# Kernel tuning notes

Measured on AMD Instinct MI355X. Metric: run time of the kernel, lower is better.

Reference implementation:

```python
import jax, jax.numpy as jnp
import numpy as np

B, S, HID, NH, HD, NL = 2, 4096, 1024, 16, 64, 128
N_ITER = 6


def setup_inputs() -> dict:
    key = jax.random.key(0)
    ks = jax.random.split(key, 9)
    s = 0.02
    D = NH * HD
    return {
        "X": jax.random.normal(ks[0], (B, S, HID), jnp.float32),
        "mask": jnp.ones((B, S), jnp.float32),
        "Wq": jax.random.normal(ks[1], (HID, D), jnp.float32) * s,
        "bq": jnp.zeros((D,), jnp.float32),
        "Wk": jax.random.normal(ks[2], (HID, D), jnp.float32) * s,
        "bk": jnp.zeros((D,), jnp.float32),
        "Wv": jax.random.normal(ks[3], (HID, D), jnp.float32) * s,
        "bv": jnp.zeros((D,), jnp.float32),
        "Wo": jax.random.normal(ks[4], (D, HID), jnp.float32) * s,
        "bo": jnp.zeros((HID,), jnp.float32),
    }


def iterative_inv(mat, n_iter=N_ITER):
    # Newton-Schulz style pseudo-inverse iteration (Nystromformer 'original' init)
    I = jnp.eye(mat.shape[-1], dtype=mat.dtype)
    K = mat
    V = K.swapaxes(-1, -2) / jnp.max(jnp.sum(K, axis=-2))
    for _ in range(n_iter):
        KV = K @ V
        V = 0.25 * V @ (13.0 * I - KV @ (15.0 * I - KV @ (7.0 * I - KV)))
    return V


def nystrom_core(Q, K, V, mask):
    # Q,K,V: [B,NH,S,HD], mask: [B,S]
    scale = 1.0 / np.sqrt(np.sqrt(HD))  # 1/d^(1/4) applied to both Q and K
    m = mask[:, None, :, None]
    Q = Q * m * scale
    K = K * m * scale
    seg = S // NL
    # landmarks: mean over contiguous segments -> [B,NH,NL,HD]
    Ql = Q.reshape(B, NH, NL, seg, HD).mean(axis=-2)
    Kl = K.reshape(B, NH, NL, seg, HD).mean(axis=-2)
    k1 = jax.nn.softmax(jnp.einsum('bhsd,bhld->bhsl', Q, Kl), axis=-1)   # [B,NH,S,NL]
    k2 = jax.nn.softmax(jnp.einsum('bhld,bhmd->bhlm', Ql, Kl), axis=-1)  # [B,NH,NL,NL]
    k3 = jax.nn.softmax(
        jnp.einsum('bhld,bhsd->bhls', Ql, K) - 1e9 * (1.0 - mask[:, None, None, :]),
        axis=-1)                                                          # [B,NH,NL,S]
    return k1 @ iterative_inv(k2) @ (k3 @ V)                              # [B,NH,S,HD]


def reference(X, mask, Wq, bq, Wk, bk, Wv, bv, Wo, bo):
    def split(Y):  # [B,S,NH*HD] -> [B,NH,S,HD]
        return Y.reshape(B, S, NH, HD).transpose(0, 2, 1, 3)
    Q = split(X @ Wq + bq)
    K = split(X @ Wk + bk)
    V = split(X @ Wv + bv)
    attn = nystrom_core(Q.astype(jnp.float32), K.astype(jnp.float32),
                        V.astype(jnp.float32), mask.astype(jnp.float32))
    out = attn.transpose(0, 2, 1, 3).reshape(B, S, NH * HD)
    return out @ Wo + bo
```

## Files before the change

### kernel.cpp

```cpp
#include <hip/hip_runtime.h>
#include <math.h>

constexpr int cB = 2, cS = 4096, cHID = 1024, cNH = 16, cHD = 64, cNL = 128, cSEG = 32, cD = 1024, cBH = 32;
constexpr float cSCALE = 0.35355339059327373f;

typedef _Float16 f16x8 __attribute__((ext_vector_type(8)));
typedef float f32x4 __attribute__((ext_vector_type(4)));

__device__ inline void gload_lds16(const void* g, void* l) {
    __builtin_amdgcn_global_load_lds(
        (const __attribute__((address_space(1))) void*)g,
        (__attribute__((address_space(3))) void*)l, 16, 0, 0);
}

__global__ __launch_bounds__(256) void cast_x(const float* __restrict__ X, _Float16* __restrict__ Xh)
{
    int i = (blockIdx.x * 256 + threadIdx.x) * 4;
    float4 v = *reinterpret_cast<const float4*>(X + i);
    union { _Float16 h[4]; ushort4 u; } p;
    p.h[0] = (_Float16)v.x; p.h[1] = (_Float16)v.y; p.h[2] = (_Float16)v.z; p.h[3] = (_Float16)v.w;
    *reinterpret_cast<ushort4*>(Xh + i) = p.u;
}

__global__ __launch_bounds__(256) void wcast_t(
    const float* __restrict__ Wq, const float* __restrict__ Wk,
    const float* __restrict__ Wv, const float* __restrict__ Wo,
    _Float16* __restrict__ WqT, _Float16* __restrict__ WkT,
    _Float16* __restrict__ WvT, _Float16* __restrict__ WoT)
{
    __shared__ float tile[32][33];
    const int wsel = blockIdx.z;
    const float* W = (wsel == 0) ? Wq : (wsel == 1 ? Wk : (wsel == 2 ? Wv : Wo));
    _Float16* WT   = (wsel == 0) ? WqT : (wsel == 1 ? WkT : (wsel == 2 ? WvT : WoT));
    const int n0 = blockIdx.x * 32, k0 = blockIdx.y * 32;
    const int t = threadIdx.x;
    const int r = t >> 3, c = (t & 7) * 4;
    float4 v = *reinterpret_cast<const float4*>(W + (size_t)(k0 + r) * cD + n0 + c);
    tile[r][c] = v.x; tile[r][c + 1] = v.y; tile[r][c + 2] = v.z; tile[r][c + 3] = v.w;
    __syncthreads();
    union { _Float16 h[4]; ushort4 u; } p;
    p.h[0] = (_Float16)tile[c + 0][r]; p.h[1] = (_Float16)tile[c + 1][r];
    p.h[2] = (_Float16)tile[c + 2][r]; p.h[3] = (_Float16)tile[c + 3][r];
    *reinterpret_cast<ushort4*>(WT + (size_t)(n0 + r) * cHID + k0 + c) = p.u;
}

__global__ __launch_bounds__(256) void xm_kernel(
    const float* __restrict__ X, const float* __restrict__ mask,
    float* __restrict__ Xm, float* __restrict__ mbar)
{
    const int bl = blockIdx.x;
    const int b = bl >> 7, l = bl & 127;
    const int c = threadIdx.x * 4;
    float4 a = {0.f, 0.f, 0.f, 0.f};
    float msum = 0.f;
    for (int j = 0; j < cSEG; ++j) {
        float m = mask[b * cS + l * cSEG + j];
        float4 x = *reinterpret_cast<const float4*>(X + ((size_t)(b * cS + l * cSEG + j)) * cHID + c);
        a.x += m * x.x; a.y += m * x.y; a.z += m * x.z; a.w += m * x.w;
        msum += m;
    }
    const float inv = 1.0f / cSEG;
    a.x *= inv; a.y *= inv; a.z *= inv; a.w *= inv;
    *reinterpret_cast<float4*>(Xm + (size_t)bl * cHID + c) = a;
    if (threadIdx.x == 0) mbar[bl] = msum * inv;
}

__global__ __launch_bounds__(256) void qkv_gemm_f16(
    const _Float16* __restrict__ Xh, const float* __restrict__ mask,
    const _Float16* __restrict__ WqT, const _Float16* __restrict__ WkT, const _Float16* __restrict__ WvT,
    const float* __restrict__ bq, const float* __restrict__ bk, const float* __restrict__ bv,
    _Float16* __restrict__ Qh, _Float16* __restrict__ Kh, _Float16* __restrict__ Vh)
{
    __shared__ __align__(16) _Float16 As[128 * 64];
    __shared__ __align__(16) _Float16 Bs[128 * 64];
    const int wsel = blockIdx.z;
    const _Float16* WT = (wsel == 0) ? WqT : (wsel == 1 ? WkT : WvT);
    const float* bias  = (wsel == 0) ? bq  : (wsel == 1 ? bk  : bv);
    _Float16* Y        = (wsel == 0) ? Qh  : (wsel == 1 ? Kh  : Vh);
    const int n0 = blockIdx.x * 128, m0 = blockIdx.y * 128;
    const int t = threadIdx.x;
    const int wave = t >> 6, lane = t & 63;
    const int wm = (wave >> 1) * 64, wn = (wave & 1) * 64;
    const int quad = lane >> 4, l15 = lane & 15;
    const int srow = wave * 8 + (lane >> 3);
    const int scol = (lane & 7) * 8;

    f32x4 acc[4][4];
#pragma unroll
    for (int i = 0; i < 4; ++i)
#pragma unroll
        for (int j = 0; j < 4; ++j) acc[i][j] = (f32x4){0.f, 0.f, 0.f, 0.f};

    for (int k0 = 0; k0 < cHID; k0 += 64) {
        const _Float16* aSrc = Xh + (size_t)(m0 + srow) * cHID + k0 + scol;
        const _Float16* bSrc = WT + (size_t)(n0 + srow) * cHID + k0 + scol;
#pragma unroll
        for (int i = 0; i < 4; ++i) {
            gload_lds16(aSrc + (size_t)(i * 32) * cHID, &As[(wave * 8 + i * 32) * 64]);
            gload_lds16(bSrc + (size_t)(i * 32) * cHID, &Bs[(wave * 8 + i * 32) * 64]);
        }
        __syncthreads();
        f16x8 af[2][4], bf[2][4];
#pragma unroll
        for (int kh = 0; kh < 2; ++kh) {
#pragma unroll
            for (int mt = 0; mt < 4; ++mt)
                af[kh][mt] = *reinterpret_cast<const f16x8*>(&As[(wm + mt * 16 + l15) * 64 + kh * 32 + quad * 8]);
#pragma unroll
            for (int nt = 0; nt < 4; ++nt)
                bf[kh][nt] = *reinterpret_cast<const f16x8*>(&Bs[(wn + nt * 16 + l15) * 64 + kh * 32 + quad * 8]);
        }
#pragma unroll
        for (int kh = 0; kh < 2; ++kh)
#pragma unroll
            for (int mt = 0; mt < 4; ++mt)
#pragma unroll
                for (int nt = 0; nt < 4; ++nt)
                    acc[mt][nt] = __builtin_amdgcn_mfma_f32_16x16x32_f16(af[kh][mt], bf[kh][nt], acc[mt][nt], 0, 0, 0);
        __syncthreads();
    }
#pragma unroll
    for (int mt = 0; mt < 4; ++mt) {
#pragma unroll
        for (int r = 0; r < 4; ++r) {
            int R = m0 + wm + mt * 16 + quad * 4 + r;
            int b = R >> 12, s = R & (cS - 1);
            float msc = (wsel < 2) ? mask[b * cS + s] * cSCALE : 1.0f;
#pragma unroll
            for (int nt = 0; nt < 4; ++nt) {
                int Cc = n0 + wn + nt * 16 + l15;
                int h = Cc >> 6, d = Cc & 63;
                float val = (acc[mt][nt][r] + bias[Cc]) * msc;
                Y[((size_t)(b * cNH + h) * cS + s) * cHD + d] = (_Float16)val;
            }
        }
    }
}

__global__ __launch_bounds__(256) void out_gemm_f16(
    const _Float16* __restrict__ Ah, const _Float16* __restrict__ WT,
    const float* __restrict__ bias, float* __restrict__ Y)
{
    __shared__ __align__(16) _Float16 As[128 * 64];
    __shared__ __align__(16) _Float16 Bs[128 * 64];
    const int n0 = blockIdx.x * 128, m0 = blockIdx.y * 128;
    const int t = threadIdx.x;
    const int wave = t >> 6, lane = t & 63;
    const int wm = (wave >> 1) * 64, wn = (wave & 1) * 64;
    const int quad = lane >> 4, l15 = lane & 15;
    const int srow = wave * 8 + (lane >> 3);
    const int scol = (lane & 7) * 8;

    f32x4 acc[4][4];
#pragma unroll
    for (int i = 0; i < 4; ++i)
#pragma unroll
        for (int j = 0; j < 4; ++j) acc[i][j] = (f32x4){0.f, 0.f, 0.f, 0.f};

    for (int k0 = 0; k0 < cD; k0 += 64) {
        const _Float16* aSrc = Ah + (size_t)(m0 + srow) * cD + k0 + scol;
        const _Float16* bSrc = WT + (size_t)(n0 + srow) * cD + k0 + scol;
#pragma unroll
        for (int i = 0; i < 4; ++i) {
            gload_lds16(aSrc + (size_t)(i * 32) * cD, &As[(wave * 8 + i * 32) * 64]);
            gload_lds16(bSrc + (size_t)(i * 32) * cD, &Bs[(wave * 8 + i * 32) * 64]);
        }
        __syncthreads();
        f16x8 af[2][4], bf[2][4];
#pragma unroll
        for (int kh = 0; kh < 2; ++kh) {
#pragma unroll
            for (int mt = 0; mt < 4; ++mt)
                af[kh][mt] = *reinterpret_cast<const f16x8*>(&As[(wm + mt * 16 + l15) * 64 + kh * 32 + quad * 8]);
#pragma unroll
            for (int nt = 0; nt < 4; ++nt)
                bf[kh][nt] = *reinterpret_cast<const f16x8*>(&Bs[(wn + nt * 16 + l15) * 64 + kh * 32 + quad * 8]);
        }
#pragma unroll
        for (int kh = 0; kh < 2; ++kh)
#pragma unroll
            for (int mt = 0; mt < 4; ++mt)
#pragma unroll
                for (int nt = 0; nt < 4; ++nt)
                    acc[mt][nt] = __builtin_amdgcn_mfma_f32_16x16x32_f16(af[kh][mt], bf[kh][nt], acc[mt][nt], 0, 0, 0);
        __syncthreads();
    }
#pragma unroll
    for (int mt = 0; mt < 4; ++mt) {
#pragma unroll
        for (int r = 0; r < 4; ++r) {
            int R = m0 + wm + mt * 16 + quad * 4 + r;
#pragma unroll
            for (int nt = 0; nt < 4; ++nt) {
                int Cc = n0 + wn + nt * 16 + l15;
                Y[(size_t)R * cHID + Cc] = acc[mt][nt][r] + bias[Cc];
            }
        }
    }
}

__global__ __launch_bounds__(256) void lgemm(
    const float* __restrict__ Xm, const float* __restrict__ mbar,
    const float* __restrict__ Wq, const float* __restrict__ bq,
    const float* __restrict__ Wk, const float* __restrict__ bk,
    float* __restrict__ Ql, float* __restrict__ Kl,
    _Float16* __restrict__ Qlh, _Float16* __restrict__ Klh)
{
    __shared__ __align__(16) float As[16][68];
    __shared__ __align__(16) float Bs[16][68];
    const int tid = threadIdx.x;
    const int wsel = blockIdx.z;
    const float* W    = wsel ? Wk : Wq;
    const float* bias = wsel ? bk : bq;
    float* Yl         = wsel ? Kl : Ql;
    _Float16* Ylh     = wsel ? Klh : Qlh;
    const int c0 = blockIdx.x * 64, r0 = blockIdx.y * 64;
    const int tx = tid & 15, ty = tid >> 4;
    const int am = tid >> 2, ak = (tid & 3) * 4;
    const int bkk = tid >> 4, bn = (tid & 15) * 4;

    float acc[4][4] = {};
    for (int k0 = 0; k0 < cHID; k0 += 16) {
        float4 a4 = *reinterpret_cast<const float4*>(Xm + (size_t)(r0 + am) * cHID + k0 + ak);
        As[ak + 0][am] = a4.x; As[ak + 1][am] = a4.y; As[ak + 2][am] = a4.z; As[ak + 3][am] = a4.w;
        float4 b4 = *reinterpret_cast<const float4*>(W + (size_t)(k0 + bkk) * cD + c0 + bn);
        *reinterpret_cast<float4*>(&Bs[bkk][bn]) = b4;
        __syncthreads();
#pragma unroll
        for (int kk = 0; kk < 16; ++kk) {
            float4 av  = *reinterpret_cast<const float4*>(&As[kk][ty * 4]);
            float4 bv4 = *reinterpret_cast<const float4*>(&Bs[kk][tx * 4]);
            float a_[4] = {av.x, av.y, av.z, av.w};
            float b_[4] = {bv4.x, bv4.y, bv4.z, bv4.w};
#pragma unroll
            for (int i = 0; i < 4; ++i)
#pragma unroll
                for (int j = 0; j < 4; ++j) acc[i][j] += a_[i] * b_[j];
        }
        __syncthreads();
    }
#pragma unroll
    for (int i = 0; i < 4; ++i) {
        int r = r0 + ty * 4 + i;
        int b = r >> 7, l = r & 127;
        float mb = mbar[r];
#pragma unroll
        for (int j = 0; j < 4; ++j) {
            int c = c0 + tx * 4 + j;
            int h = c >> 6, d = c & 63;
            float val = (acc[i][j] + mb * bias[c]) * cSCALE;
            size_t idx = ((size_t)(b * cNH + h) * cNL + l) * cHD + d;
            Yl[idx] = val;
            Ylh[idx] = (_Float16)val;
        }
    }
}

__global__ __launch_bounds__(128) void k2_softmax(
    const float* __restrict__ Ql, const float* __restrict__ Kl, float* __restrict__ k2)
{
    __shared__ __align__(16) float qrow[64];
    __shared__ float red[128];
    int bh = blockIdx.x >> 7, i = blockIdx.x & 127;
    int j = threadIdx.x;
    if (j < 64) qrow[j] = Ql[(bh * cNL + i) * cHD + j];
    __syncthreads();
    const float4* q4  = reinterpret_cast<const float4*>(qrow);
    const float4* kl4 = reinterpret_cast<const float4*>(Kl + (bh * cNL + j) * cHD);
    float dot = 0.f;
#pragma unroll
    for (int u = 0; u < 16; ++u) {
        float4 a = q4[u], b = kl4[u];
        dot += a.x * b.x + a.y * b.y + a.z * b.z + a.w * b.w;
    }
    red[j] = dot; __syncthreads();
    for (int off = 64; off > 0; off >>= 1) { if (j < off) red[j] = fmaxf(red[j], red[j + off]); __syncthreads(); }
    float m = red[0]; __syncthreads();
    float e = expf(dot - m);
    red[j] = e; __syncthreads();
    for (int off = 64; off > 0; off >>= 1) { if (j < off) red[j] += red[j + off]; __syncthreads(); }
    k2[(bh * cNL + i) * cNL + j] = e / red[0];
}

__global__ __launch_bounds__(128) void colsum_max(const float* __restrict__ k2, int* __restrict__ cmax)
{
    __shared__ float red[128];
    int bh = blockIdx.x, j = threadIdx.x;
    float s = 0.f;
    for (int i = 0; i < cNL; ++i) s += k2[(bh * cNL + i) * cNL + j];
    red[j] = s; __syncthreads();
    for (int off = 64; off > 0; off >>= 1) { if (j < off) red[j] = fmaxf(red[j], red[j + off]); __syncthreads(); }
    if (j == 0) atomicMax(cmax, __float_as_int(red[0]));
}

__device__ inline unsigned int packsplit(float v) {
    _Float16 h = (_Float16)v;
    _Float16 l = (_Float16)(v - (float)h);
    union { _Float16 f; unsigned short u; } ha, la;
    ha.f = h; la.f = l;
    return ((unsigned int)ha.u << 16) | (unsigned int)la.u;
}
__device__ inline float h2f(unsigned short u) {
    union { unsigned short u; _Float16 f; } c; c.u = u; return (float)c.f;
}

#define NYS_PRODUCT(Rbuf, LH, LL)                                                       \
    {                                                                                   \
        _Pragma("unroll")                                                               \
        for (int nt_ = 0; nt_ < 8; ++nt_) {                                             \
            f32x4 a_ = (f32x4){0.f, 0.f, 0.f, 0.f};                                     \
            _Pragma("unroll")                                                           \
            for (int k0_ = 0; k0_ < 4; ++k0_) {                                         \
                const unsigned int* p_ = Rbuf + (nt_ * 16 + l15) * 132 + k0_ * 32 + quad * 8; \
                uint4 w0_ = *reinterpret_cast<const uint4*>(p_);                        \
                uint4 w1_ = *reinterpret_cast<const uint4*>(p_ + 4);                    \
                union { f16x8 v; unsigned int u[4]; } bh_, bl_;                         \
                bh_.u[0] = (w0_.x >> 16) | (w0_.y & 0xFFFF0000u);                       \
                bh_.u[1] = (w0_.z >> 16) | (w0_.w & 0xFFFF0000u);                       \
                bh_.u[2] = (w1_.x >> 16) | (w1_.y & 0xFFFF0000u);                       \
                bh_.u[3] = (w1_.z >> 16) | (w1_.w & 0xFFFF0000u);                       \
                bl_.u[0] = (w0_.x & 0xFFFFu) | (w0_.y << 16);                           \
                bl_.u[1] = (w0_.z & 0xFFFFu) | (w0_.w << 16);                           \
                bl_.u[2] = (w1_.x & 0xFFFFu) | (w1_.y << 16);                           \
                bl_.u[3] = (w1_.z & 0xFFFFu) | (w1_.w << 16);                           \
                a_ = __builtin_amdgcn_mfma_f32_16x16x32_f16(LH[k0_], bh_.v, a_, 0, 0, 0); \
                a_ = __builtin_amdgcn_mfma_f32_16x16x32_f16(LL[k0_], bh_.v, a_, 0, 0, 0); \
                a_ = __builtin_amdgcn_mfma_f32_16x16x32_f16(LH[k0_], bl_.v, a_, 0, 0, 0); \
            }                                                                           \
            acc[nt_] = a_;                                                              \
        }                                                                               \
    }

#define NYS_SCATTER(Rbuf, alphav)                                                       \
    {                                                                                   \
        _Pragma("unroll")                                                               \
        for (int nt_ = 0; nt_ < 8; ++nt_) {                                             \
            _Pragma("unroll")                                                           \
            for (int r_ = 0; r_ < 4; ++r_) {                                            \
                int row_ = wave * 16 + quad * 4 + r_;                                   \
                int col_ = nt_ * 16 + l15;                                              \
                float v_ = -acc[nt_][r_];                                               \
                if (row_ == col_) v_ += (alphav);                                       \
                Rbuf[col_ * 132 + row_] = packsplit(v_);                                \
            }                                                                           \
        }                                                                               \
    }

__global__ __launch_bounds__(512, 2) void nys_fused(
    const float* __restrict__ k2, const int* __restrict__ cmax, float* __restrict__ V6)
{
    __shared__ __align__(16) unsigned int RT0[128 * 132];
    __shared__ __align__(16) unsigned int RT1[128 * 132];
    const int bh = blockIdx.x;
    const int t = threadIdx.x;
    const int wave = t >> 6, lane = t & 63;
    const int quad = lane >> 4, l15 = lane & 15;
    const int rowL = wave * 16 + l15;
    const float* Kg = k2 + (size_t)bh * (cNL * cNL);
    const float invc = 1.0f / __int_as_float(*cmax);

#pragma unroll
    for (int i = 0; i < 32; ++i) {
        int idx = t + i * 512;
        RT0[(idx >> 7) * 132 + (idx & 127)] = packsplit(Kg[idx] * invc);
    }

    f16x8 Khi[4], Klo[4];
#pragma unroll
    for (int k0 = 0; k0 < 4; ++k0) {
        const float* src = Kg + (size_t)rowL * cNL + k0 * 32 + quad * 8;
        union { f16x8 v; unsigned short s[8]; } hh, ll;
#pragma unroll
        for (int j = 0; j < 8; ++j) {
            float v = src[j];
            _Float16 h = (_Float16)v;
            _Float16 l = (_Float16)(v - (float)h);
            union { _Float16 f; unsigned short u; } cb;
            cb.f = h; hh.s[j] = cb.u;
            cb.f = l; ll.s[j] = cb.u;
        }
        Khi[k0] = hh.v; Klo[k0] = ll.v;
    }
    __syncthreads();

    f32x4 acc[8];
    f16x8 Ahi[4], Alo[4], Vhi[4], Vlo[4];

    for (int it = 0; it < 6; ++it) {
        NYS_PRODUCT(RT0, Khi, Klo);
        __syncthreads();
        NYS_SCATTER(RT1, 7.0f);
        __syncthreads();

#pragma unroll
        for (int k0 = 0; k0 < 4; ++k0) {
            union { f16x8 v; unsigned short s[8]; } hh, ll;
#pragma unroll
            for (int j = 0; j < 8; ++j) {
                int kk = k0 * 32 + quad * 8 + j;
                unsigned int u = RT1[kk * 132 + rowL];
                float val = h2f((unsigned short)(u >> 16)) + h2f((unsigned short)(u & 0xFFFFu));
                float a = (kk == rowL) ? (7.0f - val) : (-val);
                _Float16 h = (_Float16)a;
                _Float16 l = (_Float16)(a - (float)h);
                union { _Float16 f; unsigned short u2; } cb;
                cb.f = h; hh.s[j] = cb.u2;
                cb.f = l; ll.s[j] = cb.u2;
            }
            Ahi[k0] = hh.v; Alo[k0] = ll.v;
        }

        NYS_PRODUCT(RT1, Ahi, Alo);
        __syncthreads();
        NYS_SCATTER(RT1, 15.0f);
        __syncthreads();

        NYS_PRODUCT(RT1, Ahi, Alo);

#pragma unroll
        for (int k0 = 0; k0 < 4; ++k0) {
            union { f16x8 v; unsigned short s[8]; } hh, ll;
#pragma unroll
            for (int j = 0; j < 8; ++j) {
                unsigned int u = RT0[(k0 * 32 + quad * 8 + j) * 132 + rowL];
                hh.s[j] = (unsigned short)(u >> 16);
                ll.s[j] = (unsigned short)(u & 0xFFFFu);
            }
            Vhi[k0] = hh.v; Vlo[k0] = ll.v;
        }
        __syncthreads();
        NYS_SCATTER(RT1, 13.0f);
        __syncthreads();

        NYS_PRODUCT(RT1, Vhi, Vlo);
        if (it < 5) {
            __syncthreads();
#pragma unroll
            for (int nt = 0; nt < 8; ++nt)
#pragma unroll
                for (int r = 0; r < 4; ++r) {
                    int row = wave * 16 + quad * 4 + r;
                    int col = nt * 16 + l15;
                    RT0[col * 132 + row] = packsplit(0.25f * acc[nt][r]);
                }
            __syncthreads();
        }
    }
#pragma unroll
    for (int nt = 0; nt < 8; ++nt)
#pragma unroll
        for (int r = 0; r < 4; ++r) {
            int row = wave * 16 + quad * 4 + r;
            int col = nt * 16 + l15;
            V6[(size_t)bh * (cNL * cNL) + row * cNL + col] = 0.25f * acc[nt][r];
        }
}

__global__ __launch_bounds__(256) void vtrans(const _Float16* __restrict__ Vh, _Float16* __restrict__ VTh)
{
    __shared__ ushort T[64][72];
    const int s0 = blockIdx.x * 64, bh = blockIdx.y;
    const int t = threadIdx.x;
    const _Float16* vb = Vh + ((size_t)bh * cS + s0) * cHD;
#pragma unroll
    for (int i = 0; i < 2; ++i) {
        int idx = t + i * 256;
        int row = idx >> 3, c8 = idx & 7;
        f16x8 v = *reinterpret_cast<const f16x8*>(vb + (size_t)row * cHD + c8 * 8);
#pragma unroll
        for (int j = 0; j < 8; ++j) T[row][c8 * 8 + j] = ((ushort*)&v)[j];
    }
    __syncthreads();
    _Float16* vt = VTh + (size_t)bh * cHD * cS;
#pragma unroll
    for (int i = 0; i < 2; ++i) {
        int idx = t + i * 256;
        int d = idx >> 3, s8 = idx & 7;
        f16x8 o;
#pragma unroll
        for (int j = 0; j < 8; ++j) ((ushort*)&o)[j] = T[s8 * 8 + j][d];
        *reinterpret_cast<f16x8*>(vt + (size_t)d * cS + s0 + s8 * 8) = o;
    }
}

__global__ __launch_bounds__(256) void k3v_mfma(
    const _Float16* __restrict__ Qlh, const _Float16* __restrict__ Kh,
    const _Float16* __restrict__ VTh, const float* __restrict__ mask,
    float* __restrict__ Opart, float* __restrict__ mpart, float* __restrict__ spart)
{
    __shared__ __align__(16) _Float16 Ps[128 * 72];
    __shared__ float msk[256];
    const int z = blockIdx.x, bh = blockIdx.y;
    const int b = bh >> 4;
    const int sbase = z * 256;
    const int t = threadIdx.x;
    const int wave = t >> 6, lane = t & 63;
    const int quad = lane >> 4, l15 = lane & 15;

    msk[t] = mask[b * cS + sbase + t];

    f16x8 aq[2][2];
    const _Float16* qlg = Qlh + (size_t)bh * cNL * cHD;
#pragma unroll
    for (int mt = 0; mt < 2; ++mt)
#pragma unroll
        for (int k0 = 0; k0 < 2; ++k0)
            aq[mt][k0] = *reinterpret_cast<const f16x8*>(
                qlg + (size_t)(wave * 32 + mt * 16 + l15) * cHD + k0 * 32 + quad * 8);

    float mrun[2][4], srun[2][4];
    f32x4 accO[2][4];
#pragma unroll
    for (int mt = 0; mt < 2; ++mt)
#pragma unroll
        for (int r = 0; r < 4; ++r) { mrun[mt][r] = -1e30f; srun[mt][r] = 0.f; }
#pragma unroll
    for (int mt = 0; mt < 2; ++mt)
#pragma unroll
        for (int dt = 0; dt < 4; ++dt) accO[mt][dt] = (f32x4){0.f, 0.f, 0.f, 0.f};

    __syncthreads();

    const _Float16* kg = Kh + (size_t)bh * cS * cHD;
    const _Float16* vg = VTh + (size_t)bh * cHD * cS;

    for (int step = 0; step < 4; ++step) {
        const int st = sbase + step * 64;
        f32x4 accS[2][4];
#pragma unroll
        for (int mt = 0; mt < 2; ++mt)
#pragma unroll
            for (int nt = 0; nt < 4; ++nt) accS[mt][nt] = (f32x4){0.f, 0.f, 0.f, 0.f};
#pragma unroll
        for (int k0 = 0; k0 < 2; ++k0)
#pragma unroll
            for (int nt = 0; nt < 4; ++nt) {
                f16x8 bk = *reinterpret_cast<const f16x8*>(
                    kg + (size_t)(st + nt * 16 + l15) * cHD + k0 * 32 + quad * 8);
#pragma unroll
                for (int mt = 0; mt < 2; ++mt)
                    accS[mt][nt] = __builtin_amdgcn_mfma_f32_16x16x32_f16(aq[mt][k0], bk, accS[mt][nt], 0, 0, 0);
            }
#pragma unroll
        for (int nt = 0; nt < 4; ++nt) {
            float pen = 1e9f * (1.0f - msk[step * 64 + nt * 16 + l15]);
#pragma unroll
            for (int mt = 0; mt < 2; ++mt)
#pragma unroll
                for (int r = 0; r < 4; ++r) accS[mt][nt][r] -= pen;
        }
#pragma unroll
        for (int mt = 0; mt < 2; ++mt) {
#pragma unroll
            for (int r = 0; r < 4; ++r) {
                float tmax = fmaxf(fmaxf(accS[mt][0][r], accS[mt][1][r]),
                                   fmaxf(accS[mt][2][r], accS[mt][3][r]));
#pragma unroll
                for (int w = 1; w < 16; w <<= 1) tmax = fmaxf(tmax, __shfl_xor(tmax, w, 16));
                float mnew = fmaxf(mrun[mt][r], tmax);
                float alpha = __expf(mrun[mt][r] - mnew);
                float ts = 0.f;
#pragma unroll
                for (int nt = 0; nt < 4; ++nt) {
                    float e = __expf(accS[mt][nt][r] - mnew);
                    accS[mt][nt][r] = e; ts += e;
                }
#pragma unroll
                for (int w = 1; w < 16; w <<= 1) ts += __shfl_xor(ts, w, 16);
                srun[mt][r] = srun[mt][r] * alpha + ts;
                mrun[mt][r] = mnew;
#pragma unroll
                for (int dt = 0; dt < 4; ++dt) accO[mt][dt][r] *= alpha;
            }
        }
#pragma unroll
        for (int mt = 0; mt < 2; ++mt)
#pragma unroll
            for (int nt = 0; nt < 4; ++nt)
#pragma unroll
                for (int r = 0; r < 4; ++r)
                    Ps[(wave * 32 + mt * 16 + quad * 4 + r) * 72 + nt * 16 + l15] =
                        (_Float16)accS[mt][nt][r];
#pragma unroll
        for (int k0 = 0; k0 < 2; ++k0) {
            f16x8 ap[2];
#pragma unroll
            for (int mt = 0; mt < 2; ++mt)
                ap[mt] = *reinterpret_cast<const f16x8*>(
                    &Ps[(wave * 32 + mt * 16 + l15) * 72 + k0 * 32 + quad * 8]);
#pragma unroll
            for (int dt = 0; dt < 4; ++dt) {
                f16x8 bv = *reinterpret_cast<const f16x8*>(
                    vg + (size_t)(dt * 16 + l15) * cS + st + k0 * 32 + quad * 8);
#pragma unroll
                for (int mt = 0; mt < 2; ++mt)
                    accO[mt][dt] = __builtin_amdgcn_mfma_f32_16x16x32_f16(ap[mt], bv, accO[mt][dt], 0, 0, 0);
            }
        }
    }
    const int rowbase = bh * cNL + wave * 32;
#pragma unroll
    for (int mt = 0; mt < 2; ++mt)
#pragma unroll
        for (int dt = 0; dt < 4; ++dt)
#pragma unroll
            for (int r = 0; r < 4; ++r)
                Opart[(size_t)(z * 4096 + rowbase + mt * 16 + quad * 4 + r) * cHD + dt * 16 + l15] =
                    accO[mt][dt][r];
    if (l15 == 0) {
#pragma unroll
        for (int mt = 0; mt < 2; ++mt)
#pragma unroll
            for (int r = 0; r < 4; ++r) {
                int prow = z * 4096 + rowbase + mt * 16 + quad * 4 + r;
                mpart[prow] = mrun[mt][r];
                spart[prow] = srun[mt][r];
            }
    }
}

__global__ __launch_bounds__(256) void k3v_reduce(
    const float* __restrict__ Opart, const float* __restrict__ mpart,
    const float* __restrict__ spart, float* __restrict__ CV)
{
    const int t = threadIdx.x;
    const int row = blockIdx.x * 4 + (t >> 6);
    const int d = t & 63;
    float mstar = -1e30f;
#pragma unroll
    for (int z = 0; z < 16; ++z) mstar = fmaxf(mstar, mpart[z * 4096 + row]);
    float ssum = 0.f, acc = 0.f;
#pragma unroll
    for (int z = 0; z < 16; ++z) {
        float w = __expf(mpart[z * 4096 + row] - mstar);
        ssum += w * spart[z * 4096 + row];
        acc  += w * Opart[(size_t)(z * 4096 + row) * cHD + d];
    }
    CV[(size_t)row * cHD + d] = acc / ssum;
}

__global__ __launch_bounds__(256) void w2_matmul(
    const float* __restrict__ V6, const float* __restrict__ CV, _Float16* __restrict__ W2T)
{
    __shared__ __align__(16) float CVs[128][64];
    const int bh = blockIdx.x, t = threadIdx.x;
    for (int k = 0; k < 32; ++k) { int idx = t + k * 256; CVs[idx >> 6][idx & 63] = CV[bh * 8192 + idx]; }
    __syncthreads();
    const int tx = t & 15, ty = t >> 4;
    float acc[8][4] = {};
    for (int k = 0; k < 128; ++k) {
        float4 b4 = *reinterpret_cast<const float4*>(&CVs[k][tx * 4]);
#pragma unroll
        for (int i = 0; i < 8; ++i) {
            float a = V6[(bh * cNL + ty * 8 + i) * cNL + k];
            acc[i][0] += a * b4.x; acc[i][1] += a * b4.y; acc[i][2] += a * b4.z; acc[i][3] += a * b4.w;
        }
    }
    _Float16* wt = W2T + (size_t)bh * cHD * cNL;
#pragma unroll
    for (int i = 0; i < 8; ++i)
#pragma unroll
        for (int j = 0; j < 4; ++j)
            wt[(size_t)(tx * 4 + j) * cNL + ty * 8 + i] = (_Float16)acc[i][j];
}

__global__ __launch_bounds__(256) void k1_mfma(
    const _Float16* __restrict__ Qh, const _Float16* __restrict__ Klh,
    const _Float16* __restrict__ W2T, _Float16* __restrict__ ctxh)
{
    __shared__ __align__(16) _Float16 Qs[64 * 72];
    __shared__ __align__(16) _Float16 Ps[64 * 136];
    const int s0 = blockIdx.x * 64, bh = blockIdx.y;
    const int b = bh >> 4, h = bh & 15;
    const int t = threadIdx.x;
    const int wave = t >> 6, lane = t & 63;
    const int quad = lane >> 4, l15 = lane & 15;

    {
        const _Float16* qg = Qh + ((size_t)bh * cS + s0) * cHD;
#pragma unroll
        for (int i = 0; i < 2; ++i) {
            int idx = t + i * 256;
            int row = idx >> 3, c8 = idx & 7;
            *reinterpret_cast<f16x8*>(&Qs[row * 72 + c8 * 8]) =
                *reinterpret_cast<const f16x8*>(qg + (size_t)row * cHD + c8 * 8);
        }
    }
    __syncthreads();

    const _Float16* klg = Klh + (size_t)bh * cNL * cHD;
    f32x4 accS[8];
#pragma unroll
    for (int nt = 0; nt < 8; ++nt) accS[nt] = (f32x4){0.f, 0.f, 0.f, 0.f};
#pragma unroll
    for (int k0 = 0; k0 < 2; ++k0) {
        f16x8 aq = *reinterpret_cast<const f16x8*>(&Qs[(wave * 16 + l15) * 72 + k0 * 32 + quad * 8]);
#pragma unroll
        for (int nt = 0; nt < 8; ++nt) {
            f16x8 bk = *reinterpret_cast<const f16x8*>(klg + (size_t)(nt * 16 + l15) * cHD + k0 * 32 + quad * 8);
            accS[nt] = __builtin_amdgcn_mfma_f32_16x16x32_f16(aq, bk, accS[nt], 0, 0, 0);
        }
    }

    float rmax[4] = {-1e30f, -1e30f, -1e30f, -1e30f};
#pragma unroll
    for (int nt = 0; nt < 8; ++nt)
#pragma unroll
        for (int r = 0; r < 4; ++r) rmax[r] = fmaxf(rmax[r], accS[nt][r]);
#pragma unroll
    for (int r = 0; r < 4; ++r)
#pragma unroll
        for (int w = 1; w < 16; w <<= 1) rmax[r] = fmaxf(rmax[r], __shfl_xor(rmax[r], w, 16));
    float rsum[4] = {0.f, 0.f, 0.f, 0.f};
#pragma unroll
    for (int nt = 0; nt < 8; ++nt)
#pragma unroll
        for (int r = 0; r < 4; ++r) { accS[nt][r] = __expf(accS[nt][r] - rmax[r]); rsum[r] += accS[nt][r]; }
#pragma unroll
    for (int r = 0; r < 4; ++r) {
#pragma unroll
        for (int w = 1; w < 16; w <<= 1) rsum[r] += __shfl_xor(rsum[r], w, 16);
        rsum[r] = 1.0f / rsum[r];
    }
#pragma unroll
    for (int nt = 0; nt < 8; ++nt)
#pragma unroll
        for (int r = 0; r < 4; ++r)
            Ps[(wave * 16 + quad * 4 + r) * 136 + nt * 16 + l15] = (_Float16)(accS[nt][r] * rsum[r]);
    __syncthreads();

    const _Float16* wtg = W2T + (size_t)bh * cHD * cNL;
    f32x4 accO[4];
#pragma unroll
    for (int nt = 0; nt < 4; ++nt) accO[nt] = (f32x4){0.f, 0.f, 0.f, 0.f};
#pragma unroll
    for (int k0 = 0; k0 < 4; ++k0) {
        f16x8 ap = *reinterpret_cast<const f16x8*>(&Ps[(wave * 16 + l15) * 136 + k0 * 32 + quad * 8]);
#pragma unroll
        for (int nt = 0; nt < 4; ++nt) {
            f16x8 bw = *reinterpret_cast<const f16x8*>(wtg + (size_t)(nt * 16 + l15) * cNL + k0 * 32 + quad * 8);
            accO[nt] = __builtin_amdgcn_mfma_f32_16x16x32_f16(ap, bw, accO[nt], 0, 0, 0);
        }
    }
#pragma unroll
    for (int nt = 0; nt < 4; ++nt)
#pragma unroll
        for (int r = 0; r < 4; ++r) {
            int s = s0 + wave * 16 + quad * 4 + r;
            int d = nt * 16 + l15;
            ctxh[((size_t)(b * cS) + s) * cD + h * cHD + d] = (_Float16)accO[nt][r];
        }
}

extern "C" void kernel_launch(void* const* d_in, const int* in_sizes, int n_in,
                              void* d_out, int out_size, void* d_ws, size_t ws_size,
                              hipStream_t stream)
{
    const float* X    = (const float*)d_in[0];
    const float* mask = (const float*)d_in[1];
    const float* Wq   = (const float*)d_in[2];
    const float* bq   = (const float*)d_in[3];
    const float* Wk   = (const float*)d_in[4];
    const float* bk   = (const float*)d_in[5];
    const float* Wv   = (const float*)d_in[6];
    const float* bv   = (const float*)d_in[7];
    const float* Wo   = (const float*)d_in[8];
    const float* bo   = (const float*)d_in[9];
    float* out = (float*)d_out;

    float* ws = (float*)d_ws;
    size_t off = 0;
    const size_t szQKV = (size_t)cBH * cS * cHD;
    const size_t szL   = (size_t)cBH * cNL * cHD;
    const size_t szM   = (size_t)cBH * cNL * cNL;
    float* Qr   = ws + off; off += szQKV;
    float* Kr   = ws + off; off += szQKV;
    float* Vr   = ws + off; off += szQKV;
    _Float16* Xh  = (_Float16*)(ws + off); off += szQKV / 2;
    _Float16* WqT = (_Float16*)(ws + off); off += 524288;
    _Float16* WkT = (_Float16*)(ws + off); off += 524288;
    _Float16* WvT = (_Float16*)(ws + off); off += 524288;
    _Float16* WoT = (_Float16*)(ws + off); off += 524288;
    float* Xm   = ws + off; off += (size_t)cB * cNL * cHID;
    float* mbar = ws + off; off += 256;
    float* Ql  = ws + off; off += szL;
    float* Kl  = ws + off; off += szL;
    float* k2  = ws + off; off += szM;
    float* Vb0 = ws + off; off += szM;
    float* Vb1 = ws + off; off += szM;
    float* Zb  = ws + off; off += szM;
    float* T2b = ws + off; off += szM;
    float* T3b = ws + off; off += szM;
    float* CV  = ws + off; off += szL;
    _Float16* Qlh  = (_Float16*)(ws + off); off += szL / 2;
    _Float16* Klh  = (_Float16*)(ws + off); off += szL / 2;
    _Float16* W2Th = (_Float16*)(ws + off); off += szL / 2;
    int*   cmax = (int*)(ws + off); off += 16;
    float* mpart = ws + off; off += 65536;
    float* spart = ws + off; off += 65536;

    _Float16* Qh   = (_Float16*)Qr;
    float*    Opart = Qr + szQKV / 2;
    _Float16* Kh   = (_Float16*)Kr;
    _Float16* ctxh = (_Float16*)(Kr + szQKV / 2);
    _Float16* Vh   = (_Float16*)Vr;
    _Float16* VTh  = (_Float16*)(Vr + szQKV / 2);

    (void)Vb1; (void)Zb; (void)T2b; (void)T3b;

    hipMemsetAsync(cmax, 0, sizeof(int), stream);

    cast_x<<<(int)(szQKV / 1024), 256, 0, stream>>>(X, Xh);
    wcast_t<<<dim3(32, 32, 4), 256, 0, stream>>>(Wq, Wk, Wv, Wo, WqT, WkT, WvT, WoT);
    xm_kernel<<<cB * cNL, 256, 0, stream>>>(X, mask, Xm, mbar);

    qkv_gemm_f16<<<dim3(cD / 128, (cB * cS) / 128, 3), 256, 0, stream>>>(
        Xh, mask, WqT, WkT, WvT, bq, bk, bv, Qh, Kh, Vh);
    vtrans<<<dim3(cS / 64, cBH), 256, 0, stream>>>(Vh, VTh);
    lgemm<<<dim3(cD / 64, (cB * cNL) / 64, 2), 256, 0, stream>>>(Xm, mbar, Wq, bq, Wk, bk, Ql, Kl, Qlh, Klh);

    k2_softmax<<<cBH * cNL, 128, 0, stream>>>(Ql, Kl, k2);
    colsum_max<<<cBH, 128, 0, stream>>>(k2, cmax);

    nys_fused<<<cBH, 512, 0, stream>>>(k2, cmax, Vb0);

    k3v_mfma<<<dim3(16, cBH), 256, 0, stream>>>(Qlh, Kh, VTh, mask, Opart, mpart, spart);
    k3v_reduce<<<1024, 256, 0, stream>>>(Opart, mpart, spart, CV);
    w2_matmul<<<cBH, 256, 0, stream>>>(Vb0, CV, W2Th);
    k1_mfma<<<dim3(cS / 64, cBH), 256, 0, stream>>>(Qh, Klh, W2Th, ctxh);
    out_gemm_f16<<<dim3(cHID / 128, (cB * cS) / 128), 256, 0, stream>>>(ctxh, WoT, bo, out);
}
```

Baseline: 514.1 us.

## Restructure Newton-Schulz kernel: split hi/lo LDS planes, 4 waves with 2 M-tiles

The fused Newton-Schulz inverse kernel now keeps the fp16 hi and lo parts in separate LDS arrays instead of packed 32-bit words, so B operands load directly as f16x8 and no longer need per-element unpacking. It runs 256 threads where each wave owns two 16-row tiles, with two independent accumulator chains interleaved to keep more MFMAs in flight. Scatter writes are vectorized ushort4 stores, and one barrier after the first product is dropped because the first product reads a different buffer. Fewer waves per block and more registers per wave may reduce latency hiding, and this kernel runs on only 32 blocks.

```diff
diff --git a/kernel.cpp b/kernel.cpp
--- a/kernel.cpp
+++ b/kernel.cpp
@@ -293,167 +293,184 @@
     if (j == 0) atomicMax(cmax, __float_as_int(red[0]));
 }
 
-__device__ inline unsigned int packsplit(float v) {
-    _Float16 h = (_Float16)v;
-    _Float16 l = (_Float16)(v - (float)h);
-    union { _Float16 f; unsigned short u; } ha, la;
-    ha.f = h; la.f = l;
-    return ((unsigned int)ha.u << 16) | (unsigned int)la.u;
-}
-__device__ inline float h2f(unsigned short u) {
-    union { unsigned short u; _Float16 f; } c; c.u = u; return (float)c.f;
-}
-
-#define NYS_PRODUCT(Rbuf, LH, LL)                                                       \
+__device__ inline void split2(float v, _Float16& h, _Float16& l) {
+    h = (_Float16)v;
+    l = (_Float16)(v - (float)h);
+}
+
+#define NYS_MFMA(a, b, c) __builtin_amdgcn_mfma_f32_16x16x32_f16((a), (b), (c), 0, 0, 0)
+
+#define NYS_PRODUCT(PH, PL, LH, LL)                                                     \
     {                                                                                   \
         _Pragma("unroll")                                                               \
         for (int nt_ = 0; nt_ < 8; ++nt_) {                                             \
-            f32x4 a_ = (f32x4){0.f, 0.f, 0.f, 0.f};                                     \
+            f32x4 a0_ = (f32x4){0.f, 0.f, 0.f, 0.f};                                    \
+            f32x4 a1_ = (f32x4){0.f, 0.f, 0.f, 0.f};                                    \
             _Pragma("unroll")                                                           \
             for (int k0_ = 0; k0_ < 4; ++k0_) {                                         \
-                const unsigned int* p_ = Rbuf + (nt_ * 16 + l15) * 132 + k0_ * 32 + quad * 8; \
-                uint4 w0_ = *reinterpret_cast<const uint4*>(p_);                        \
-                uint4 w1_ = *reinterpret_cast<const uint4*>(p_ + 4);                    \
-                union { f16x8 v; unsigned int u[4]; } bh_, bl_;                         \
-                bh_.u[0] = (w0_.x >> 16) | (w0_.y & 0xFFFF0000u);                       \
-                bh_.u[1] = (w0_.z >> 16) | (w0_.w & 0xFFFF0000u);                       \
-                bh_.u[2] = (w1_.x >> 16) | (w1_.y & 0xFFFF0000u);                       \
-                bh_.u[3] = (w1_.z >> 16) | (w1_.w & 0xFFFF0000u);                       \
-                bl_.u[0] = (w0_.x & 0xFFFFu) | (w0_.y << 16);                           \
-                bl_.u[1] = (w0_.z & 0xFFFFu) | (w0_.w << 16);                           \
-                bl_.u[2] = (w1_.x & 0xFFFFu) | (w1_.y << 16);                           \
-                bl_.u[3] = (w1_.z & 0xFFFFu) | (w1_.w << 16);                           \
-                a_ = __builtin_amdgcn_mfma_f32_16x16x32_f16(LH[k0_], bh_.v, a_, 0, 0, 0); \
-                a_ = __builtin_amdgcn_mfma_f32_16x16x32_f16(LL[k0_], bh_.v, a_, 0, 0, 0); \
-                a_ = __builtin_amdgcn_mfma_f32_16x16x32_f16(LH[k0_], bl_.v, a_, 0, 0, 0); \
+                f16x8 bh_ = *reinterpret_cast<const f16x8*>(&PH[(nt_ * 16 + l15) * 136 + k0_ * 32 + quad * 8]); \
+                f16x8 bl_ = *reinterpret_cast<const f16x8*>(&PL[(nt_ * 16 + l15) * 136 + k0_ * 32 + quad * 8]); \
+                a0_ = NYS_MFMA(LH[0][k0_], bh_, a0_);                                   \
+                a1_ = NYS_MFMA(LH[1][k0_], bh_, a1_);                                   \
+                a0_ = NYS_MFMA(LL[0][k0_], bh_, a0_);                                   \
+                a1_ = NYS_MFMA(LL[1][k0_], bh_, a1_);                                   \
+                a0_ = NYS_MFMA(LH[0][k0_], bl_, a0_);                                   \
+                a1_ = NYS_MFMA(LH[1][k0_], bl_, a1_);                                   \
             }                                                                           \
-            acc[nt_] = a_;                                                              \
+            acc[0][nt_] = a0_; acc[1][nt_] = a1_;                                       \
         }                                                                               \
     }
 
-#define NYS_SCATTER(Rbuf, alphav)                                                       \
+#define NYS_SCATTER_W(alphav)                                                           \
     {                                                                                   \
         _Pragma("unroll")                                                               \
-        for (int nt_ = 0; nt_ < 8; ++nt_) {                                             \
+        for (int mt_ = 0; mt_ < 2; ++mt_) {                                             \
             _Pragma("unroll")                                                           \
-            for (int r_ = 0; r_ < 4; ++r_) {                                            \
-                int row_ = wave * 16 + quad * 4 + r_;                                   \
+            for (int nt_ = 0; nt_ < 8; ++nt_) {                                         \
                 int col_ = nt_ * 16 + l15;                                              \
-                float v_ = -acc[nt_][r_];                                               \
-                if (row_ == col_) v_ += (alphav);                                       \
-                Rbuf[col_ * 132 + row_] = packsplit(v_);                                \
+                int rb_  = wave * 32 + mt_ * 16 + quad * 4;                             \
+                ushort4 ph_, pl_;                                                       \
+                _Pragma("unroll")                                                       \
+                for (int r_ = 0; r_ < 4; ++r_) {                                        \
+                    float v_ = ((rb_ + r_) == col_ ? (alphav) : 0.f) - acc[mt_][nt_][r_]; \
+                    _Float16 h_, l_; split2(v_, h_, l_);                                \
+                    ((unsigned short*)&ph_)[r_] = __builtin_bit_cast(unsigned short, h_); \
+                    ((unsigned short*)&pl_)[r_] = __builtin_bit_cast(unsigned short, l_); \
+                }                                                                       \
+                *reinterpret_cast<ushort4*>(&Whi_s[col_ * 136 + rb_]) = ph_;            \
+                *reinterpret_cast<ushort4*>(&Wlo_s[col_ * 136 + rb_]) = pl_;            \
             }                                                                           \
         }                                                                               \
     }
 
-__global__ __launch_bounds__(512, 2) void nys_fused(
+__global__ __launch_bounds__(256, 1) void nys_fused(
     const float* __restrict__ k2, const int* __restrict__ cmax, float* __restrict__ V6)
 {
-    __shared__ __align__(16) unsigned int RT0[128 * 132];
-    __shared__ __align__(16) unsigned int RT1[128 * 132];
+    __shared__ __align__(16) _Float16 Vhi_s[128 * 136];
+    __shared__ __align__(16) _Float16 Vlo_s[128 * 136];
+    __shared__ __align__(16) _Float16 Whi_s[128 * 136];
+    __shared__ __align__(16) _Float16 Wlo_s[128 * 136];
     const int bh = blockIdx.x;
     const int t = threadIdx.x;
     const int wave = t >> 6, lane = t & 63;
     const int quad = lane >> 4, l15 = lane & 15;
-    const int rowL = wave * 16 + l15;
     const float* Kg = k2 + (size_t)bh * (cNL * cNL);
     const float invc = 1.0f / __int_as_float(*cmax);
 
 #pragma unroll
-    for (int i = 0; i < 32; ++i) {
-        int idx = t + i * 512;
-        RT0[(idx >> 7) * 132 + (idx & 127)] = packsplit(Kg[idx] * invc);
-    }
-
-    f16x8 Khi[4], Klo[4];
-#pragma unroll
-    for (int k0 = 0; k0 < 4; ++k0) {
-        const float* src = Kg + (size_t)rowL * cNL + k0 * 32 + quad * 8;
-        union { f16x8 v; unsigned short s[8]; } hh, ll;
-#pragma unroll
-        for (int j = 0; j < 8; ++j) {
-            float v = src[j];
-            _Float16 h = (_Float16)v;
-            _Float16 l = (_Float16)(v - (float)h);
-            union { _Float16 f; unsigned short u; } cb;
-            cb.f = h; hh.s[j] = cb.u;
-            cb.f = l; ll.s[j] = cb.u;
-        }
-        Khi[k0] = hh.v; Klo[k0] = ll.v;
+    for (int i = 0; i < 16; ++i) {
+        int idx = t + i * 256;
+        int row = idx >> 5, c4 = (idx & 31) * 4;
+        float4 v = *reinterpret_cast<const float4*>(Kg + (size_t)row * cNL + c4);
+        ushort4 ph, pl;
+        _Float16 h, l;
+        split2(v.x * invc, h, l); ((unsigned short*)&ph)[0] = __builtin_bit_cast(unsigned short, h); ((unsigned short*)&pl)[0] = __builtin_bit_cast(unsigned short, l);
+        split2(v.y * invc, h, l); ((unsigned short*)&ph)[1] = __builtin_bit_cast(unsigned short, h); ((unsigned short*)&pl)[1] = __builtin_bit_cast(unsigned short, l);
+        split2(v.z * invc, h, l); ((unsigned short*)&ph)[2] = __builtin_bit_cast(unsigned short, h); ((unsigned short*)&pl)[2] = __builtin_bit_cast(unsigned short, l);
+        split2(v.w * invc, h, l); ((unsigned short*)&ph)[3] = __builtin_bit_cast(unsigned short, h); ((unsigned short*)&pl)[3] = __builtin_bit_cast(unsigned short, l);
+        *reinterpret_cast<ushort4*>(&Vhi_s[row * 136 + c4]) = ph;
+        *reinterpret_cast<ushort4*>(&Vlo_s[row * 136 + c4]) = pl;
+    }
+
+    f16x8 Khi[2][4], Klo[2][4];
+#pragma unroll
+    for (int mt = 0; mt < 2; ++mt) {
+        const int rowL = wave * 32 + mt * 16 + l15;
+#pragma unroll
+        for (int k0 = 0; k0 < 4; ++k0) {
+            const float* src = Kg + (size_t)rowL * cNL + k0 * 32 + quad * 8;
+            union { f16x8 v; _Float16 e[8]; } hh, ll;
+#pragma unroll
+            for (int j = 0; j < 8; ++j) split2(src[j], hh.e[j], ll.e[j]);
+            Khi[mt][k0] = hh.v; Klo[mt][k0] = ll.v;
+        }
     }
     __syncthreads();
 
-    f32x4 acc[8];
-    f16x8 Ahi[4], Alo[4], Vhi[4], Vlo[4];
+    f32x4 acc[2][8];
+    f16x8 Ahi[2][4], Alo[2][4];
 
     for (int it = 0; it < 6; ++it) {
-        NYS_PRODUCT(RT0, Khi, Klo);
-        __syncthreads();
-        NYS_SCATTER(RT1, 7.0f);
-        __syncthreads();
-
-#pragma unroll
-        for (int k0 = 0; k0 < 4; ++k0) {
-            union { f16x8 v; unsigned short s[8]; } hh, ll;
-#pragma unroll
-            for (int j = 0; j < 8; ++j) {
-                int kk = k0 * 32 + quad * 8 + j;
-                unsigned int u = RT1[kk * 132 + rowL];
-                float val = h2f((unsigned short)(u >> 16)) + h2f((unsigned short)(u & 0xFFFFu));
-                float a = (kk == rowL) ? (7.0f - val) : (-val);
-                _Float16 h = (_Float16)a;
-                _Float16 l = (_Float16)(a - (float)h);
-                union { _Float16 f; unsigned short u2; } cb;
-                cb.f = h; hh.s[j] = cb.u2;
-                cb.f = l; ll.s[j] = cb.u2;
-            }
-            Ahi[k0] = hh.v; Alo[k0] = ll.v;
-        }
-
-        NYS_PRODUCT(RT1, Ahi, Alo);
-        __syncthreads();
-        NYS_SCATTER(RT1, 15.0f);
-        __syncthreads();
-
-        NYS_PRODUCT(RT1, Ahi, Alo);
-
-#pragma unroll
-        for (int k0 = 0; k0 < 4; ++k0) {
-            union { f16x8 v; unsigned short s[8]; } hh, ll;
-#pragma unroll
-            for (int j = 0; j < 8; ++j) {
-                unsigned int u = RT0[(k0 * 32 + quad * 8 + j) * 132 + rowL];
-                hh.s[j] = (unsigned short)(u >> 16);
-                ll.s[j] = (unsigned short)(u & 0xFFFFu);
-            }
-            Vhi[k0] = hh.v; Vlo[k0] = ll.v;
-        }
-        __syncthreads();
-        NYS_SCATTER(RT1, 13.0f);
-        __syncthreads();
-
-        NYS_PRODUCT(RT1, Vhi, Vlo);
+        NYS_PRODUCT(Vhi_s, Vlo_s, Khi, Klo);
+        NYS_SCATTER_W(7.0f);
+        __syncthreads();
+
+#pragma unroll
+        for (int mt = 0; mt < 2; ++mt) {
+            const int rowL = wave * 32 + mt * 16 + l15;
+#pragma unroll
+            for (int k0 = 0; k0 < 4; ++k0) {
+                union { f16x8 v; _Float16 e[8]; } hh, ll;
+#pragma unroll
+                for (int j = 0; j < 8; ++j) {
+                    int kk = k0 * 32 + quad * 8 + j;
+                    float s = (float)Whi_s[kk * 136 + rowL] + (float)Wlo_s[kk * 136 + rowL];
+                    float a = ((kk == rowL) ? 7.0f : 0.0f) - s;
+                    split2(a, hh.e[j], ll.e[j]);
+                }
+                Ahi[mt][k0] = hh.v; Alo[mt][k0] = ll.v;
+            }
+        }
+
+        NYS_PRODUCT(Whi_s, Wlo_s, Ahi, Alo);
+        __syncthreads();
+        NYS_SCATTER_W(15.0f);
+        __syncthreads();
+
+        NYS_PRODUCT(Whi_s, Wlo_s, Ahi, Alo);
+
+        f16x8 Vlh[2][4], Vll[2][4];
+#pragma unroll
+        for (int mt = 0; mt < 2; ++mt) {
+            const int rowL = wave * 32 + mt * 16 + l15;
+#pragma unroll
+            for (int k0 = 0; k0 < 4; ++k0) {
+                union { f16x8 v; _Float16 e[8]; } hh, ll;
+#pragma unroll
+                for (int j = 0; j < 8; ++j) {
+                    int kk = k0 * 32 + quad * 8 + j;
+                    hh.e[j] = Vhi_s[kk * 136 + rowL];
+                    ll.e[j] = Vlo_s[kk * 136 + rowL];
+                }
+                Vlh[mt][k0] = hh.v; Vll[mt][k0] = ll.v;
+            }
+        }
+        __syncthreads();
+        NYS_SCATTER_W(13.0f);
+        __syncthreads();
+
+        NYS_PRODUCT(Whi_s, Wlo_s, Vlh, Vll);
         if (it < 5) {
+#pragma unroll
+            for (int mt = 0; mt < 2; ++mt) {
+#pragma unroll
+                for (int nt = 0; nt < 8; ++nt) {
+                    int col = nt * 16 + l15;
+                    int rb  = wave * 32 + mt * 16 + quad * 4;
+                    ushort4 ph, pl;
+#pragma unroll
+                    for (int r = 0; r < 4; ++r) {
+                        _Float16 h, l; split2(0.25f * acc[mt][nt][r], h, l);
+                        ((unsigned short*)&ph)[r] = __builtin_bit_cast(unsigned short, h);
+                        ((unsigned short*)&pl)[r] = __builtin_bit_cast(unsigned short, l);
+                    }
+                    *reinterpret_cast<ushort4*>(&Vhi_s[col * 136 + rb]) = ph;
+                    *reinterpret_cast<ushort4*>(&Vlo_s[col * 136 + rb]) = pl;
+                }
+            }
             __syncthreads();
-#pragma unroll
-            for (int nt = 0; nt < 8; ++nt)
-#pragma unroll
-                for (int r = 0; r < 4; ++r) {
-                    int row = wave * 16 + quad * 4 + r;
-                    int col = nt * 16 + l15;
-                    RT0[col * 132 + row] = packsplit(0.25f * acc[nt][r]);
-                }
-            __syncthreads();
-        }
-    }
-#pragma unroll
-    for (int nt = 0; nt < 8; ++nt)
-#pragma unroll
-        for (int r = 0; r < 4; ++r) {
-            int row = wave * 16 + quad * 4 + r;
-            int col = nt * 16 + l15;
-            V6[(size_t)bh * (cNL * cNL) + row * cNL + col] = 0.25f * acc[nt][r];
-        }
+        }
+    }
+#pragma unroll
+    for (int mt = 0; mt < 2; ++mt)
+#pragma unroll
+        for (int nt = 0; nt < 8; ++nt)
+#pragma unroll
+            for (int r = 0; r < 4; ++r) {
+                int row = wave * 32 + mt * 16 + quad * 4 + r;
+                int col = nt * 16 + l15;
+                V6[(size_t)bh * (cNL * cNL) + row * cNL + col] = 0.25f * acc[mt][nt][r];
+            }
 }
 
 __global__ __launch_bounds__(256) void vtrans(const _Float16* __restrict__ Vh, _Float16* __restrict__ VTh)
@@ -822,7 +839,7 @@
     k2_softmax<<<cBH * cNL, 128, 0, stream>>>(Ql, Kl, k2);
     colsum_max<<<cBH, 128, 0, stream>>>(k2, cmax);
 
-    nys_fused<<<cBH, 512, 0, stream>>>(k2, cmax, Vb0);
+    nys_fused<<<cBH, 256, 0, stream>>>(k2, cmax, Vb0);
 
     k3v_mfma<<<dim3(16, cBH), 256, 0, stream>>>(Qlh, Kh, VTh, mask, Opart, mpart, spart);
     k3v_reduce<<<1024, 256, 0, stream>>>(Opart, mpart, spart, CV);
```

Result: slower. 556.1 us (+8.2%).
